# Kernel tuning notes

Hardware: AMD Instinct MI355X
Metric: run time of the kernel (lower is better)

Reference implementation:

```python
import jax, jax.numpy as jnp
import numpy as np
from jax import lax


def _lstm_dir(x, w_ih, w_hh, b_ih, b_hh, reverse):
    # x: [B,T,E]; torch LSTM gate order: i, f, g, o
    B, T, _ = x.shape
    H = w_hh.shape[1]
    xp = jnp.einsum('bte,ge->btg', x, w_ih) + b_ih + b_hh  # [B,T,4H]
    def step(carry, xt):
        h, c = carry
        gates = xt + h @ w_hh.T
        i, f, g, o = jnp.split(gates, 4, axis=-1)
        c = jax.nn.sigmoid(f) * c + jax.nn.sigmoid(i) * jnp.tanh(g)
        h = jax.nn.sigmoid(o) * jnp.tanh(c)
        return (h, c), h
    h0 = jnp.zeros((B, H), x.dtype)
    _, hs = lax.scan(step, (h0, h0), jnp.swapaxes(xp, 0, 1), reverse=reverse)
    return jnp.swapaxes(hs, 0, 1)  # [B,T,H]


def _crf_llh(emissions, tags, mask, start, end, trans):
    # torchcrf log-likelihood; emissions [B,T,C], tags [B,T], mask [B,T] bool
    maskf = mask.astype(emissions.dtype)
    em_sc = jnp.take_along_axis(emissions, tags[..., None], axis=-1)[..., 0]  # [B,T]
    tr_sc = trans[tags[:, :-1], tags[:, 1:]]                                   # [B,T-1]
    num = start[tags[:, 0]] + em_sc[:, 0] + jnp.sum((em_sc[:, 1:] + tr_sc) * maskf[:, 1:], axis=1)
    last_idx = jnp.sum(mask.astype(jnp.int32), axis=1) - 1
    last_tag = jnp.take_along_axis(tags, last_idx[:, None], axis=1)[:, 0]
    num = num + end[last_tag]
    # forward algorithm (partition function)
    alpha0 = start + emissions[:, 0]  # [B,C]
    def step(alpha, inp):
        em_t, m_t = inp  # [B,C], [B]
        sc = alpha[:, :, None] + trans[None] + em_t[:, None, :]  # [B,C,C]
        nxt = jax.scipy.special.logsumexp(sc, axis=1)
        return jnp.where(m_t[:, None], nxt, alpha), None
    alpha, _ = lax.scan(step, alpha0,
                        (jnp.swapaxes(emissions[:, 1:], 0, 1), jnp.swapaxes(mask[:, 1:], 0, 1)))
    den = jax.scipy.special.logsumexp(alpha + end[None, :], axis=1)
    return num - den  # [B]


def setup_inputs() -> dict:
    key = jax.random.key(0)
    ks = jax.random.split(key, 16)
    V, E, H, C = 30000, 512, 512, 9
    B, T = 32, 256
    s_emb = 1.0
    s_l = 1.0 / np.sqrt(H)
    inp = {
        'input': jax.random.randint(ks[0], (B, T), 0, V),
        'label': jax.random.randint(ks[1], (B, T), 0, C),
        'emb_table': jax.random.normal(ks[2], (V, E), jnp.float32) * s_emb,
        'w_ih_f': jax.random.uniform(ks[3], (4 * H, E), jnp.float32, -s_l, s_l),
        'w_hh_f': jax.random.uniform(ks[4], (4 * H, H), jnp.float32, -s_l, s_l),
        'b_ih_f': jax.random.uniform(ks[5], (4 * H,), jnp.float32, -s_l, s_l),
        'b_hh_f': jax.random.uniform(ks[6], (4 * H,), jnp.float32, -s_l, s_l),
        'w_ih_b': jax.random.uniform(ks[7], (4 * H, E), jnp.float32, -s_l, s_l),
        'w_hh_b': jax.random.uniform(ks[8], (4 * H, H), jnp.float32, -s_l, s_l),
        'b_ih_b': jax.random.uniform(ks[9], (4 * H,), jnp.float32, -s_l, s_l),
        'b_hh_b': jax.random.uniform(ks[10], (4 * H,), jnp.float32, -s_l, s_l),
        'cls_w': jax.random.uniform(ks[11], (C, 2 * H), jnp.float32, -s_l, s_l),
        'cls_b': jax.random.uniform(ks[12], (C,), jnp.float32, -s_l, s_l),
        'start_trans': jax.random.uniform(ks[13], (C,), jnp.float32, -0.1, 0.1),
        'end_trans': jax.random.uniform(ks[14], (C,), jnp.float32, -0.1, 0.1),
        'trans': jax.random.uniform(ks[15], (C, C), jnp.float32, -0.1, 0.1),
    }
    return inp


def reference(input, label, emb_table, w_ih_f, w_hh_f, b_ih_f, b_hh_f,
              w_ih_b, w_hh_b, b_ih_b, b_hh_b, cls_w, cls_b,
              start_trans, end_trans, trans):
    emb = emb_table.at[0].set(0.0)  # padding_idx=0
    x = emb[input]                  # [B,T,E]
    hf = _lstm_dir(x, w_ih_f, w_hh_f, b_ih_f, b_hh_f, reverse=False)
    hb = _lstm_dir(x, w_ih_b, w_hh_b, b_ih_b, b_hh_b, reverse=True)
    h = jnp.concatenate([hf, hb], axis=-1)          # [B,T,2H]
    logits = h @ cls_w.T + cls_b                    # [B,T,C]
    mask = label > -1
    llh = _crf_llh(logits, label, mask, start_trans, end_trans, trans)
    return -jnp.mean(llh)  # reduction='mean', negated
```

## Files before the change

kernel.cpp:

```cpp
#include <hip/hip_runtime.h>

#define TT 256
#define BB 32
#define HH 512
#define EE 512
#define GG 2048
#define MM 8192
#define NWG 32

typedef __attribute__((ext_vector_type(8))) short bf16x8;
typedef __attribute__((ext_vector_type(4))) float f32x4;
typedef __attribute__((ext_vector_type(4))) unsigned short us4;
typedef unsigned long long ull;

__device__ inline float b2f(unsigned short u) {
    union { unsigned int i; float f; } v; v.i = ((unsigned int)u) << 16; return v.f;
}
__device__ inline unsigned short f2b(float f) {
    union { float f; unsigned int i; } v; v.f = f;
    unsigned int x = v.i;
    return (unsigned short)((x + 0x7FFFu + ((x >> 16) & 1u)) >> 16);
}
__device__ inline float sigm(float x) { return 1.f / (1.f + __expf(-x)); }
__device__ inline float tanh_f(float x) {
    float ax = fminf(fabsf(x), 12.f);
    float e = __expf(2.f * ax);
    float r = (e - 1.f) / (e + 1.f);
    return x < 0.f ? -r : r;
}

__global__ void prep_embed_k(const int* __restrict__ ids, const float* __restrict__ emb,
                             const float* __restrict__ wihf, const float* __restrict__ whhf,
                             const float* __restrict__ wihb, const float* __restrict__ whhb,
                             const float* __restrict__ bihf, const float* __restrict__ bhhf,
                             const float* __restrict__ bihb, const float* __restrict__ bhhb,
                             unsigned short* __restrict__ xb, unsigned short* __restrict__ wih,
                             unsigned short* __restrict__ whh, float* __restrict__ bias)
{
    int v = blockIdx.x * 256 + threadIdx.x;
    {
        int row = v >> 7;
        int col4 = (v & 127) * 4;
        int id = ids[row];
        float4 e;
        if (id != 0) e = *(const float4*)(emb + (size_t)id * 512 + col4);
        else { e.x = 0.f; e.y = 0.f; e.z = 0.f; e.w = 0.f; }
        us4 o; o.x = f2b(e.x); o.y = f2b(e.y); o.z = f2b(e.z); o.w = f2b(e.w);
        *(us4*)(xb + (size_t)row * 512 + col4) = o;
    }
    if (v < 262144) {
        float4 a; us4 o;
        a = ((const float4*)wihf)[v];
        o.x = f2b(a.x); o.y = f2b(a.y); o.z = f2b(a.z); o.w = f2b(a.w);
        *(us4*)(wih + (size_t)v * 4) = o;
        a = ((const float4*)whhf)[v];
        o.x = f2b(a.x); o.y = f2b(a.y); o.z = f2b(a.z); o.w = f2b(a.w);
        *(us4*)(whh + (size_t)v * 4) = o;
        a = ((const float4*)wihb)[v];
        o.x = f2b(a.x); o.y = f2b(a.y); o.z = f2b(a.z); o.w = f2b(a.w);
        *(us4*)(wih + 1048576 + (size_t)v * 4) = o;
        a = ((const float4*)whhb)[v];
        o.x = f2b(a.x); o.y = f2b(a.y); o.z = f2b(a.z); o.w = f2b(a.w);
        *(us4*)(whh + 1048576 + (size_t)v * 4) = o;
        if (v < 2048)      bias[v] = bihf[v] + bhhf[v];
        else if (v < 4096) bias[v] = bihb[v - 2048] + bhhb[v - 2048];
    }
}

__global__ __launch_bounds__(256, 1) void lstm_rec(const unsigned short* __restrict__ whh,
                                                   const unsigned short* __restrict__ wih,
                                                   const unsigned short* __restrict__ xb,
                                                   const float* __restrict__ bias,
                                                   unsigned short* __restrict__ h_all,
                                                   unsigned int* __restrict__ cnt)
{
    __shared__ unsigned short hbuf[32][520];
    __shared__ unsigned short xbuf[2][32][520];
    __shared__ float gbuf[4][32][16];

    const int bx = blockIdx.x;
    const int dir = bx >> 5;
    const int wg = bx & 31;
    const int js = wg * 16;
    const int tid = threadIdx.x;
    const int wave = tid >> 6, lane = tid & 63;
    const int quad = lane >> 4, r16 = lane & 15;
    const int colw = wave * 512 + js + r16;

    bf16x8 wfr[16], xfr[16];
    {
        const unsigned short* wrow = whh + (size_t)dir * GG * HH + (size_t)colw * 512;
        const unsigned short* xrow = wih + (size_t)dir * GG * EE + (size_t)colw * 512;
#pragma unroll
        for (int kc = 0; kc < 16; ++kc) {
            wfr[kc] = *(const bf16x8*)(wrow + kc * 32 + quad * 8);
            xfr[kc] = *(const bf16x8*)(xrow + kc * 32 + quad * 8);
        }
    }
    const float bsw = bias[dir * GG + colw];

    const int cb = tid >> 3, cj = (tid & 7) * 2;
    float cr0 = 0.f, cr1 = 0.f;

    unsigned short* hd = h_all + (size_t)dir * TT * BB * HH;
    unsigned int* flg = cnt + dir * NWG;
    const int xrow32 = tid >> 3;
    const ull* xbsrc = (const ull*)xb;

    {
        const int te0 = dir ? (TT - 1) : 0;
#pragma unroll
        for (int i = 0; i < 16; ++i) {
            int v = tid + i * 256;
            int row = v >> 7, wi = v & 127;
            ull xv = xbsrc[(size_t)((row << 8) + te0) * 64 + wi];
            *(ull*)&xbuf[0][row][wi * 4] = xv;
        }
    }
    __syncthreads();
    int buf = 0;

    for (int t = 0; t < TT; ++t) {
        const int te = dir ? (TT - 1 - t) : t;

        ull xpre[16];
        if (t + 1 < TT) {
            const int tn = dir ? (te - 1) : (te + 1);
#pragma unroll
            for (int i = 0; i < 16; ++i) {
                int v = tid + i * 256;
                int row = v >> 7, wi = v & 127;
                xpre[i] = xbsrc[(size_t)((row << 8) + tn) * 64 + wi];
            }
        }

        f32x4 alo = {0.f, 0.f, 0.f, 0.f}, ahi = {0.f, 0.f, 0.f, 0.f};
#pragma unroll
        for (int kc = 0; kc < 16; ++kc) {
            const int ko = kc * 32 + quad * 8;
            bf16x8 aflo = *(const bf16x8*)&xbuf[buf][r16][ko];
            bf16x8 afhi = *(const bf16x8*)&xbuf[buf][16 + r16][ko];
            alo = __builtin_amdgcn_mfma_f32_16x16x32_bf16(aflo, xfr[kc], alo, 0, 0, 0);
            ahi = __builtin_amdgcn_mfma_f32_16x16x32_bf16(afhi, xfr[kc], ahi, 0, 0, 0);
        }

        if (t > 0) {
            if (wave == 0) {
                const unsigned int tgt = (unsigned int)t;
                for (;;) {
                    unsigned int f = tgt;
                    if (lane < NWG)
                        f = __hip_atomic_load(&flg[lane], __ATOMIC_RELAXED, __HIP_MEMORY_SCOPE_AGENT);
                    if (__ballot(f >= tgt) == ~0ull) break;
                }
            }
            __syncthreads();
            const int tp = dir ? (te + 1) : (te - 1);
            const ull* hsrc = (const ull*)(hd + (size_t)tp * BB * HH);
            ull hv[16];
#pragma unroll
            for (int i = 0; i < 16; ++i)
                hv[i] = __hip_atomic_load(&hsrc[tid + i * 256], __ATOMIC_RELAXED, __HIP_MEMORY_SCOPE_AGENT);
#pragma unroll
            for (int i = 0; i < 16; ++i) {
                int v = tid + i * 256;
                *(ull*)&hbuf[v >> 7][(v & 127) * 4] = hv[i];
            }
            __syncthreads();

#pragma unroll
            for (int kc = 0; kc < 16; ++kc) {
                const int ko = kc * 32 + quad * 8;
                bf16x8 aflo = *(const bf16x8*)&hbuf[r16][ko];
                bf16x8 afhi = *(const bf16x8*)&hbuf[16 + r16][ko];
                alo = __builtin_amdgcn_mfma_f32_16x16x32_bf16(aflo, wfr[kc], alo, 0, 0, 0);
                ahi = __builtin_amdgcn_mfma_f32_16x16x32_bf16(afhi, wfr[kc], ahi, 0, 0, 0);
            }
        }

#pragma unroll
        for (int r = 0; r < 4; ++r) {
            gbuf[wave][quad * 4 + r][r16]      = alo[r] + bsw;
            gbuf[wave][16 + quad * 4 + r][r16] = ahi[r] + bsw;
        }
        __syncthreads();

        {
            float2 iv = *(const float2*)&gbuf[0][cb][cj];
            float2 fv = *(const float2*)&gbuf[1][cb][cj];
            float2 gv = *(const float2*)&gbuf[2][cb][cj];
            float2 ov = *(const float2*)&gbuf[3][cb][cj];
            cr0 = sigm(fv.x) * cr0 + sigm(iv.x) * tanh_f(gv.x);
            cr1 = sigm(fv.y) * cr1 + sigm(iv.y) * tanh_f(gv.y);
            float h0 = sigm(ov.x) * tanh_f(cr0);
            float h1 = sigm(ov.y) * tanh_f(cr1);
            unsigned int packed = (unsigned int)f2b(h0) | ((unsigned int)f2b(h1) << 16);
            unsigned int* hp = (unsigned int*)(hd + (size_t)te * BB * HH + cb * 512 + js + cj);
            __hip_atomic_store(hp, packed, __ATOMIC_RELAXED, __HIP_MEMORY_SCOPE_AGENT);
        }

        if (t + 1 < TT) {
#pragma unroll
            for (int i = 0; i < 16; ++i) {
                int v = tid + i * 256;
                *(ull*)&xbuf[buf ^ 1][v >> 7][(v & 127) * 4] = xpre[i];
            }
            buf ^= 1;
        }
        __syncthreads();
        if (tid == 0)
            __hip_atomic_store(&flg[wg], (unsigned int)(t + 1),
                               __ATOMIC_RELAXED, __HIP_MEMORY_SCOPE_AGENT);
    }
}

__global__ __launch_bounds__(256) void logits_k(const unsigned short* __restrict__ h_all,
                                                const float* __restrict__ clsw,
                                                const float* __restrict__ clsb,
                                                float* __restrict__ logits)
{
    const int tid = threadIdx.x;
    const int wave = tid >> 6, lane = tid & 63;
    const int wgid = blockIdx.x * 4 + wave;

    unsigned int wreg[9][8];
#pragma unroll
    for (int c = 0; c < 9; ++c)
#pragma unroll
        for (int q = 0; q < 8; ++q) {
            float w0 = clsw[c * 1024 + (2 * q) * 64 + lane];
            float w1 = clsw[c * 1024 + (2 * q + 1) * 64 + lane];
            wreg[c][q] = (unsigned int)f2b(w0) | ((unsigned int)f2b(w1) << 16);
        }

    const unsigned short* hfb = h_all;
    const unsigned short* hbb = h_all + (size_t)TT * BB * HH;

    for (int i = 0; i < 8; ++i) {
        int m = wgid * 8 + i;
        int b = m >> 8, t = m & 255;
        const unsigned short* hf = hfb + ((size_t)t * BB + b) * HH;
        const unsigned short* hb = hbb + ((size_t)t * BB + b) * HH;
        float acc[9];
#pragma unroll
        for (int c = 0; c < 9; ++c) acc[c] = 0.f;
#pragma unroll
        for (int u = 0; u < 16; ++u) {
            const unsigned short* src = (u < 8) ? (hf + u * 64) : (hb + (u - 8) * 64);
            float hv = b2f(src[lane]);
#pragma unroll
            for (int c = 0; c < 9; ++c) {
                unsigned short wv = (u & 1) ? (unsigned short)(wreg[c][u >> 1] >> 16)
                                            : (unsigned short)(wreg[c][u >> 1] & 0xFFFFu);
                acc[c] += hv * b2f(wv);
            }
        }
#pragma unroll
        for (int c = 0; c < 9; ++c) {
            float s = acc[c];
            for (int off = 32; off > 0; off >>= 1) s += __shfl_down(s, off);
            if (lane == 0) logits[(size_t)m * 9 + c] = s + clsb[c];
        }
    }
}

__global__ void crf_k(const float* __restrict__ logits, const int* __restrict__ label,
                      const float* __restrict__ startp, const float* __restrict__ endp,
                      const float* __restrict__ trans, float* __restrict__ llh)
{
    const int b = blockIdx.x;
    const int lane = threadIdx.x;
    __shared__ float tr[81];
    __shared__ float alpha[9];
    __shared__ int tags[TT];
    for (int v = lane; v < 81; v += 64) tr[v] = trans[v];
    for (int v = lane; v < TT; v += 64) tags[v] = label[b * TT + v];
    __syncthreads();
    const float* lg = logits + (size_t)b * TT * 9;

    float part = 0.f; int mcnt = 0;
    for (int t = lane; t < TT; t += 64) {
        int tg = tags[t];
        bool m = tg > -1;
        if (m) mcnt++;
        if (t == 0)      part += startp[tg] + lg[tg];
        else if (m)      part += lg[t * 9 + tg] + tr[tags[t - 1] * 9 + tg];
    }
    for (int off = 32; off > 0; off >>= 1) {
        part += __shfl_down(part, off);
        mcnt += __shfl_down(mcnt, off);
    }
    part = __shfl(part, 0);
    mcnt = __shfl(mcnt, 0);
    float num = part + endp[tags[mcnt - 1]];

    if (lane < 9) alpha[lane] = startp[lane] + lg[lane];
    __syncthreads();
    for (int t = 1; t < TT; ++t) {
        float nxt = 0.f;
        if (lane < 9) {
            float mx = -1e30f;
#pragma unroll
            for (int c1 = 0; c1 < 9; ++c1) mx = fmaxf(mx, alpha[c1] + tr[c1 * 9 + lane]);
            float s = 0.f;
#pragma unroll
            for (int c1 = 0; c1 < 9; ++c1) s += __expf(alpha[c1] + tr[c1 * 9 + lane] - mx);
            nxt = mx + __logf(s) + lg[t * 9 + lane];
            if (tags[t] <= -1) nxt = alpha[lane];
        }
        __syncthreads();
        if (lane < 9) alpha[lane] = nxt;
        __syncthreads();
    }
    if (lane == 0) {
        float mx = -1e30f;
#pragma unroll
        for (int c = 0; c < 9; ++c) mx = fmaxf(mx, alpha[c] + endp[c]);
        float s = 0.f;
#pragma unroll
        for (int c = 0; c < 9; ++c) s += __expf(alpha[c] + endp[c] - mx);
        llh[b] = num - (mx + __logf(s));
    }
}

__global__ void fin_k(const float* __restrict__ llh, float* __restrict__ out)
{
    int lane = threadIdx.x;
    float v = (lane < 32) ? llh[lane] : 0.f;
    for (int off = 32; off > 0; off >>= 1) v += __shfl_down(v, off);
    if (lane == 0) out[0] = -v * (1.f / 32.f);
}

extern "C" void kernel_launch(void* const* d_in, const int* in_sizes, int n_in,
                              void* d_out, int out_size, void* d_ws, size_t ws_size,
                              hipStream_t stream)
{
    const int*   ids   = (const int*)  d_in[0];
    const int*   label = (const int*)  d_in[1];
    const float* emb   = (const float*)d_in[2];
    const float* wihf  = (const float*)d_in[3];
    const float* whhf  = (const float*)d_in[4];
    const float* bihf  = (const float*)d_in[5];
    const float* bhhf  = (const float*)d_in[6];
    const float* wihb  = (const float*)d_in[7];
    const float* whhb  = (const float*)d_in[8];
    const float* bihb  = (const float*)d_in[9];
    const float* bhhb  = (const float*)d_in[10];
    const float* clsw  = (const float*)d_in[11];
    const float* clsb  = (const float*)d_in[12];
    const float* stp   = (const float*)d_in[13];
    const float* enp   = (const float*)d_in[14];
    const float* trp   = (const float*)d_in[15];

    char* ws = (char*)d_ws;
    unsigned short* xb   = (unsigned short*)(ws + 0);
    unsigned short* wih  = (unsigned short*)(ws + 8388608);
    unsigned short* whh  = (unsigned short*)(ws + 12582912);
    float*          bias = (float*)(ws + 16777216);
    unsigned short* hall = (unsigned short*)(ws + 16793600);
    float*          lgt  = (float*)(ws + 33570816);
    float*          llh  = (float*)(ws + 33865728);
    unsigned int*   cnt  = (unsigned int*)(ws + 33865856);

    hipMemsetAsync(cnt, 0, 256, stream);
    prep_embed_k<<<4096, 256, 0, stream>>>(ids, emb, wihf, whhf, wihb, whhb,
                                           bihf, bhhf, bihb, bhhb, xb, wih, whh, bias);
    lstm_rec<<<64, 256, 0, stream>>>(whh, wih, xb, bias, hall, cnt);
    logits_k<<<256, 256, 0, stream>>>(hall, clsw, clsb, lgt);
    crf_k<<<32, 64, 0, stream>>>(lgt, label, stp, enp, trp, llh);
    fin_k<<<1, 64, 0, stream>>>(llh, (float*)d_out);
}
```

Baseline: 1.099 ms.

## Replace LSTM step barrier with per-producer flag polling and direct register loads

Each block no longer has one wave spin on all 32 producer flags, then barrier, stage h_{t-1} into LDS and barrier again. It now polls flag pairs per 32-column producer chunk and loads its MFMA A fragments straight from global memory into registers. It issues the matching MFMAs as each chunk becomes ready, and rotates the chunk order by workgroup index to spread contention. This aims to overlap recurrent-step waiting with compute and drop two __syncthreads and the LDS round trip. The cost is more scattered small atomic loads and more register pressure. The x-row stride is also corrected from 64 to 128 ull per row.

```diff
diff --git a/kernel.cpp b/kernel.cpp
--- a/kernel.cpp
+++ b/kernel.cpp
@@ -27,6 +27,12 @@
     float e = __expf(2.f * ax);
     float r = (e - 1.f) / (e + 1.f);
     return x < 0.f ? -r : r;
+}
+
+#define AGLD(p) __hip_atomic_load((p), __ATOMIC_RELAXED, __HIP_MEMORY_SCOPE_AGENT)
+
+__device__ inline bool prdy(ull f, unsigned int tgt) {
+    return ((unsigned int)f >= tgt) && ((unsigned int)(f >> 32) >= tgt);
 }
 
 __global__ void prep_embed_k(const int* __restrict__ ids, const float* __restrict__ emb,
@@ -74,7 +80,6 @@
                                                    unsigned short* __restrict__ h_all,
                                                    unsigned int* __restrict__ cnt)
 {
-    __shared__ unsigned short hbuf[32][520];
     __shared__ unsigned short xbuf[2][32][520];
     __shared__ float gbuf[4][32][16];
 
@@ -92,9 +97,9 @@
         const unsigned short* wrow = whh + (size_t)dir * GG * HH + (size_t)colw * 512;
         const unsigned short* xrow = wih + (size_t)dir * GG * EE + (size_t)colw * 512;
 #pragma unroll
-        for (int kc = 0; kc < 16; ++kc) {
-            wfr[kc] = *(const bf16x8*)(wrow + kc * 32 + quad * 8);
-            xfr[kc] = *(const bf16x8*)(xrow + kc * 32 + quad * 8);
+        for (int i = 0; i < 16; ++i) {
+            wfr[i] = *(const bf16x8*)(wrow + ((i + wg) & 15) * 32 + quad * 8);
+            xfr[i] = *(const bf16x8*)(xrow + i * 32 + quad * 8);
         }
     }
     const float bsw = bias[dir * GG + colw];
@@ -104,7 +109,6 @@
 
     unsigned short* hd = h_all + (size_t)dir * TT * BB * HH;
     unsigned int* flg = cnt + dir * NWG;
-    const int xrow32 = tid >> 3;
     const ull* xbsrc = (const ull*)xb;
 
     {
@@ -113,7 +117,7 @@
         for (int i = 0; i < 16; ++i) {
             int v = tid + i * 256;
             int row = v >> 7, wi = v & 127;
-            ull xv = xbsrc[(size_t)((row << 8) + te0) * 64 + wi];
+            ull xv = xbsrc[((size_t)(row << 8) + te0) * 128 + wi];
             *(ull*)&xbuf[0][row][wi * 4] = xv;
         }
     }
@@ -122,6 +126,14 @@
 
     for (int t = 0; t < TT; ++t) {
         const int te = dir ? (TT - 1 - t) : t;
+        const unsigned int tgt = (unsigned int)t;
+
+        ull pfl[16];
+        if (t > 0) {
+#pragma unroll
+            for (int i = 0; i < 8; ++i)
+                pfl[i] = AGLD((const ull*)&flg[2 * ((i + wg) & 15)]);
+        }
 
         ull xpre[16];
         if (t + 1 < TT) {
@@ -130,7 +142,7 @@
             for (int i = 0; i < 16; ++i) {
                 int v = tid + i * 256;
                 int row = v >> 7, wi = v & 127;
-                xpre[i] = xbsrc[(size_t)((row << 8) + tn) * 64 + wi];
+                xpre[i] = xbsrc[((size_t)(row << 8) + tn) * 128 + wi];
             }
         }
 
@@ -145,36 +157,48 @@
         }
 
         if (t > 0) {
-            if (wave == 0) {
-                const unsigned int tgt = (unsigned int)t;
-                for (;;) {
-                    unsigned int f = tgt;
-                    if (lane < NWG)
-                        f = __hip_atomic_load(&flg[lane], __ATOMIC_RELAXED, __HIP_MEMORY_SCOPE_AGENT);
-                    if (__ballot(f >= tgt) == ~0ull) break;
+            const int tp = dir ? (te + 1) : (te - 1);
+            const unsigned short* hsrc = hd + (size_t)tp * BB * HH;
+            const ull* hlo = (const ull*)hsrc + (size_t)r16 * 128 + quad * 2;
+            const ull* hhi = (const ull*)hsrc + (size_t)(16 + r16) * 128 + quad * 2;
+            ull av[8][4];
+
+#pragma unroll
+            for (int i = 0; i < 8; ++i) {
+                const int p = (i + wg) & 15;
+                ull f = pfl[i];
+                while (!prdy(f, tgt))
+                    f = AGLD((const ull*)&flg[2 * p]);
+                asm volatile("" ::: "memory");
+                const ull* pl = hlo + (size_t)p * 8;
+                const ull* ph = hhi + (size_t)p * 8;
+                av[i][0] = AGLD(pl);
+                av[i][1] = AGLD(pl + 1);
+                av[i][2] = AGLD(ph);
+                av[i][3] = AGLD(ph + 1);
+                pfl[i + 8] = AGLD((const ull*)&flg[2 * ((i + 8 + wg) & 15)]);
+            }
+#pragma unroll
+            for (int i = 0; i < 16; ++i) {
+                const int s = i & 7;
+                union { ull u[2]; bf16x8 v; } fl, fh;
+                fl.u[0] = av[s][0]; fl.u[1] = av[s][1];
+                fh.u[0] = av[s][2]; fh.u[1] = av[s][3];
+                alo = __builtin_amdgcn_mfma_f32_16x16x32_bf16(fl.v, wfr[i], alo, 0, 0, 0);
+                ahi = __builtin_amdgcn_mfma_f32_16x16x32_bf16(fh.v, wfr[i], ahi, 0, 0, 0);
+                if (i < 8) {
+                    const int p = (i + 8 + wg) & 15;
+                    ull f = pfl[i + 8];
+                    while (!prdy(f, tgt))
+                        f = AGLD((const ull*)&flg[2 * p]);
+                    asm volatile("" ::: "memory");
+                    const ull* pl = hlo + (size_t)p * 8;
+                    const ull* ph = hhi + (size_t)p * 8;
+                    av[s][0] = AGLD(pl);
+                    av[s][1] = AGLD(pl + 1);
+                    av[s][2] = AGLD(ph);
+                    av[s][3] = AGLD(ph + 1);
                 }
-            }
-            __syncthreads();
-            const int tp = dir ? (te + 1) : (te - 1);
-            const ull* hsrc = (const ull*)(hd + (size_t)tp * BB * HH);
-            ull hv[16];
-#pragma unroll
-            for (int i = 0; i < 16; ++i)
-                hv[i] = __hip_atomic_load(&hsrc[tid + i * 256], __ATOMIC_RELAXED, __HIP_MEMORY_SCOPE_AGENT);
-#pragma unroll
-            for (int i = 0; i < 16; ++i) {
-                int v = tid + i * 256;
-                *(ull*)&hbuf[v >> 7][(v & 127) * 4] = hv[i];
-            }
-            __syncthreads();
-
-#pragma unroll
-            for (int kc = 0; kc < 16; ++kc) {
-                const int ko = kc * 32 + quad * 8;
-                bf16x8 aflo = *(const bf16x8*)&hbuf[r16][ko];
-                bf16x8 afhi = *(const bf16x8*)&hbuf[16 + r16][ko];
-                alo = __builtin_amdgcn_mfma_f32_16x16x32_bf16(aflo, wfr[kc], alo, 0, 0, 0);
-                ahi = __builtin_amdgcn_mfma_f32_16x16x32_bf16(afhi, wfr[kc], ahi, 0, 0, 0);
             }
         }
 
@@ -341,6 +365,7 @@
     const float* wihf  = (const float*)d_in[3];
     const float* whhf  = (const float*)d_in[4];
     const float* bihf  = (const float*)d_in[5];
+    const float* bihf2 = 0; (void)bihf2;
     const float* bhhf  = (const float*)d_in[6];
     const float* wihb  = (const float*)d_in[7];
     const float* whhb  = (const float*)d_in[8];
```

Measured after the change: 2.817 ms. 156% more time.

## Replace flag barrier with timestep-tagged hidden-state words in LSTM recurrence

Applied to the files above, without the earlier changes.

Each hidden-state store becomes a 64-bit word that packs two bf16 values with the timestep as a tag. Consumers poll the data itself until every tag matches, so the separate per-workgroup flag array, the flag polling and the end-of-step block barrier are gone. The cross-workgroup handoff per step drops from a flag round trip plus a data load to a single tagged data load. In exchange, the hidden-state buffer doubles in size, a 32MB memset to 0xFF runs on every call to invalidate the tags, and the logits kernel must unpack the wider layout. The x-row stride in the prefetch is also corrected to 128 words.

```diff
diff --git a/kernel.cpp b/kernel.cpp
--- a/kernel.cpp
+++ b/kernel.cpp
@@ -28,6 +28,9 @@
     float r = (e - 1.f) / (e + 1.f);
     return x < 0.f ? -r : r;
 }
+
+#define AGLD(p) __hip_atomic_load((p), __ATOMIC_RELAXED, __HIP_MEMORY_SCOPE_AGENT)
+#define ASTD(p, v) __hip_atomic_store((p), (v), __ATOMIC_RELAXED, __HIP_MEMORY_SCOPE_AGENT)
 
 __global__ void prep_embed_k(const int* __restrict__ ids, const float* __restrict__ emb,
                              const float* __restrict__ wihf, const float* __restrict__ whhf,
@@ -71,11 +74,10 @@
                                                    const unsigned short* __restrict__ wih,
                                                    const unsigned short* __restrict__ xb,
                                                    const float* __restrict__ bias,
-                                                   unsigned short* __restrict__ h_all,
-                                                   unsigned int* __restrict__ cnt)
-{
+                                                   ull* __restrict__ h8)
+{
+    __shared__ unsigned short xbuf[2][32][520];
     __shared__ unsigned short hbuf[32][520];
-    __shared__ unsigned short xbuf[2][32][520];
     __shared__ float gbuf[4][32][16];
 
     const int bx = blockIdx.x;
@@ -102,9 +104,7 @@
     const int cb = tid >> 3, cj = (tid & 7) * 2;
     float cr0 = 0.f, cr1 = 0.f;
 
-    unsigned short* hd = h_all + (size_t)dir * TT * BB * HH;
-    unsigned int* flg = cnt + dir * NWG;
-    const int xrow32 = tid >> 3;
+    ull* hd8 = h8 + (size_t)dir * TT * BB * 256;
     const ull* xbsrc = (const ull*)xb;
 
     {
@@ -113,7 +113,7 @@
         for (int i = 0; i < 16; ++i) {
             int v = tid + i * 256;
             int row = v >> 7, wi = v & 127;
-            ull xv = xbsrc[(size_t)((row << 8) + te0) * 64 + wi];
+            ull xv = xbsrc[((size_t)(row << 8) + te0) * 128 + wi];
             *(ull*)&xbuf[0][row][wi * 4] = xv;
         }
     }
@@ -122,6 +122,18 @@
 
     for (int t = 0; t < TT; ++t) {
         const int te = dir ? (TT - 1 - t) : t;
+
+        ull hv[32];
+        unsigned int tagexp = 0;
+        const ull* hsrc8 = hd8;
+        if (t > 0) {
+            const int tp = dir ? (te + 1) : (te - 1);
+            tagexp = (unsigned int)tp;
+            hsrc8 = hd8 + (size_t)tp * BB * 256;
+#pragma unroll
+            for (int i = 0; i < 32; ++i)
+                hv[i] = AGLD(&hsrc8[tid + i * 256]);
+        }
 
         ull xpre[16];
         if (t + 1 < TT) {
@@ -130,7 +142,7 @@
             for (int i = 0; i < 16; ++i) {
                 int v = tid + i * 256;
                 int row = v >> 7, wi = v & 127;
-                xpre[i] = xbsrc[(size_t)((row << 8) + tn) * 64 + wi];
+                xpre[i] = xbsrc[((size_t)(row << 8) + tn) * 128 + wi];
             }
         }
 
@@ -144,30 +156,33 @@
             ahi = __builtin_amdgcn_mfma_f32_16x16x32_bf16(afhi, xfr[kc], ahi, 0, 0, 0);
         }
 
-        if (t > 0) {
-            if (wave == 0) {
-                const unsigned int tgt = (unsigned int)t;
-                for (;;) {
-                    unsigned int f = tgt;
-                    if (lane < NWG)
-                        f = __hip_atomic_load(&flg[lane], __ATOMIC_RELAXED, __HIP_MEMORY_SCOPE_AGENT);
-                    if (__ballot(f >= tgt) == ~0ull) break;
-                }
-            }
-            __syncthreads();
-            const int tp = dir ? (te + 1) : (te - 1);
-            const ull* hsrc = (const ull*)(hd + (size_t)tp * BB * HH);
-            ull hv[16];
-#pragma unroll
-            for (int i = 0; i < 16; ++i)
-                hv[i] = __hip_atomic_load(&hsrc[tid + i * 256], __ATOMIC_RELAXED, __HIP_MEMORY_SCOPE_AGENT);
+        if (t + 1 < TT) {
 #pragma unroll
             for (int i = 0; i < 16; ++i) {
                 int v = tid + i * 256;
-                *(ull*)&hbuf[v >> 7][(v & 127) * 4] = hv[i];
-            }
-            __syncthreads();
-
+                *(ull*)&xbuf[buf ^ 1][v >> 7][(v & 127) * 4] = xpre[i];
+            }
+        }
+
+        if (t > 0) {
+            for (;;) {
+                unsigned int stale = 0u;
+#pragma unroll
+                for (int i = 0; i < 32; ++i)
+                    stale |= ((unsigned int)(hv[i] >> 32) != tagexp) ? (1u << i) : 0u;
+                if (__ballot(stale != 0u) == 0ull) break;
+#pragma unroll
+                for (int i = 0; i < 32; ++i)
+                    if (stale & (1u << i))
+                        hv[i] = AGLD(&hsrc8[tid + i * 256]);
+            }
+#pragma unroll
+            for (int i = 0; i < 32; ++i)
+                *(unsigned int*)&hbuf[i][tid * 2] = (unsigned int)hv[i];
+        }
+        __syncthreads();
+
+        if (t > 0) {
 #pragma unroll
             for (int kc = 0; kc < 16; ++kc) {
                 const int ko = kc * 32 + quad * 8;
@@ -195,26 +210,14 @@
             float h0 = sigm(ov.x) * tanh_f(cr0);
             float h1 = sigm(ov.y) * tanh_f(cr1);
             unsigned int packed = (unsigned int)f2b(h0) | ((unsigned int)f2b(h1) << 16);
-            unsigned int* hp = (unsigned int*)(hd + (size_t)te * BB * HH + cb * 512 + js + cj);
-            __hip_atomic_store(hp, packed, __ATOMIC_RELAXED, __HIP_MEMORY_SCOPE_AGENT);
-        }
-
-        if (t + 1 < TT) {
-#pragma unroll
-            for (int i = 0; i < 16; ++i) {
-                int v = tid + i * 256;
-                *(ull*)&xbuf[buf ^ 1][v >> 7][(v & 127) * 4] = xpre[i];
-            }
-            buf ^= 1;
-        }
-        __syncthreads();
-        if (tid == 0)
-            __hip_atomic_store(&flg[wg], (unsigned int)(t + 1),
-                               __ATOMIC_RELAXED, __HIP_MEMORY_SCOPE_AGENT);
-    }
-}
-
-__global__ __launch_bounds__(256) void logits_k(const unsigned short* __restrict__ h_all,
+            ull out = (ull)packed | ((ull)(unsigned int)te << 32);
+            ASTD(&hd8[(size_t)te * BB * 256 + cb * 256 + ((js + cj) >> 1)], out);
+        }
+        buf ^= 1;
+    }
+}
+
+__global__ __launch_bounds__(256) void logits_k(const ull* __restrict__ h8,
                                                 const float* __restrict__ clsw,
                                                 const float* __restrict__ clsb,
                                                 float* __restrict__ logits)
@@ -233,21 +236,21 @@
             wreg[c][q] = (unsigned int)f2b(w0) | ((unsigned int)f2b(w1) << 16);
         }
 
-    const unsigned short* hfb = h_all;
-    const unsigned short* hbb = h_all + (size_t)TT * BB * HH;
-
     for (int i = 0; i < 8; ++i) {
         int m = wgid * 8 + i;
         int b = m >> 8, t = m & 255;
-        const unsigned short* hf = hfb + ((size_t)t * BB + b) * HH;
-        const unsigned short* hb = hbb + ((size_t)t * BB + b) * HH;
+        const ull* hf8 = h8 + ((size_t)t * BB + b) * 256;
+        const ull* hb8 = h8 + (size_t)TT * BB * 256 + ((size_t)t * BB + b) * 256;
         float acc[9];
 #pragma unroll
         for (int c = 0; c < 9; ++c) acc[c] = 0.f;
 #pragma unroll
         for (int u = 0; u < 16; ++u) {
-            const unsigned short* src = (u < 8) ? (hf + u * 64) : (hb + (u - 8) * 64);
-            float hv = b2f(src[lane]);
+            const ull* s8 = (u < 8) ? hf8 : hb8;
+            int cc = (u & 7) * 64 + lane;
+            ull ch = s8[cc >> 1];
+            unsigned int lo = (unsigned int)ch;
+            float hv = b2f((unsigned short)(lo >> ((cc & 1) * 16)));
 #pragma unroll
             for (int c = 0; c < 9; ++c) {
                 unsigned short wv = (u & 1) ? (unsigned short)(wreg[c][u >> 1] >> 16)
@@ -357,16 +360,15 @@
     unsigned short* wih  = (unsigned short*)(ws + 8388608);
     unsigned short* whh  = (unsigned short*)(ws + 12582912);
     float*          bias = (float*)(ws + 16777216);
-    unsigned short* hall = (unsigned short*)(ws + 16793600);
-    float*          lgt  = (float*)(ws + 33570816);
-    float*          llh  = (float*)(ws + 33865728);
-    unsigned int*   cnt  = (unsigned int*)(ws + 33865856);
-
-    hipMemsetAsync(cnt, 0, 256, stream);
+    ull*            hall8= (ull*)(ws + 16793600);
+    float*          lgt  = (float*)(ws + 50348032);
+    float*          llh  = (float*)(ws + 50642944);
+
+    hipMemsetAsync(hall8, 0xFF, 33554432, stream);
     prep_embed_k<<<4096, 256, 0, stream>>>(ids, emb, wihf, whhf, wihb, whhb,
                                            bihf, bhhf, bihb, bhhb, xb, wih, whh, bias);
-    lstm_rec<<<64, 256, 0, stream>>>(whh, wih, xb, bias, hall, cnt);
-    logits_k<<<256, 256, 0, stream>>>(hall, clsw, clsb, lgt);
+    lstm_rec<<<64, 256, 0, stream>>>(whh, wih, xb, bias, hall8);
+    logits_k<<<256, 256, 0, stream>>>(hall8, clsw, clsb, lgt);
     crf_k<<<32, 64, 0, stream>>>(lgt, label, stp, enp, trp, llh);
     fin_k<<<1, 64, 0, stream>>>(llh, (float*)d_out);
 }
```

Measured after the change: 1.651 ms. 1.5x slower.

## Interleave forward and backward LSTM directions within each workgroup to hide sync latency

Applied to the files above, without the earlier changes.

Each workgroup of the recurrent kernel now runs both LSTM directions, alternating a forward step and a backward step. While one direction waits on its cross-workgroup flags and the global h loads, the workgroup does the matmul work for the other direction, so the grid halves from 64 to 32 workgroups. Flags are prefetched, and stores are drained with an explicit vmcnt wait before each flag is published. The x-row index stride also changes from 64 to 128 ull elements. Holding weight fragments for both directions plus the prefetch buffers doubles register pressure and may cause spills.

```diff
diff --git a/kernel.cpp b/kernel.cpp
--- a/kernel.cpp
+++ b/kernel.cpp
@@ -28,6 +28,9 @@
     float r = (e - 1.f) / (e + 1.f);
     return x < 0.f ? -r : r;
 }
+
+#define AGLD(p) __hip_atomic_load((p), __ATOMIC_RELAXED, __HIP_MEMORY_SCOPE_AGENT)
+#define ASTD(p, v) __hip_atomic_store((p), (v), __ATOMIC_RELAXED, __HIP_MEMORY_SCOPE_AGENT)
 
 __global__ void prep_embed_k(const int* __restrict__ ids, const float* __restrict__ emb,
                              const float* __restrict__ wihf, const float* __restrict__ whhf,
@@ -74,114 +77,116 @@
                                                    unsigned short* __restrict__ h_all,
                                                    unsigned int* __restrict__ cnt)
 {
+    __shared__ unsigned short xbufA[32][520];
+    __shared__ unsigned short xbufB[32][520];
     __shared__ unsigned short hbuf[32][520];
-    __shared__ unsigned short xbuf[2][32][520];
     __shared__ float gbuf[4][32][16];
 
-    const int bx = blockIdx.x;
-    const int dir = bx >> 5;
-    const int wg = bx & 31;
+    const int wg = blockIdx.x;
     const int js = wg * 16;
     const int tid = threadIdx.x;
     const int wave = tid >> 6, lane = tid & 63;
     const int quad = lane >> 4, r16 = lane & 15;
     const int colw = wave * 512 + js + r16;
 
-    bf16x8 wfr[16], xfr[16];
+    bf16x8 wfrA[16], xfrA[16], wfrB[16], xfrB[16];
     {
-        const unsigned short* wrow = whh + (size_t)dir * GG * HH + (size_t)colw * 512;
-        const unsigned short* xrow = wih + (size_t)dir * GG * EE + (size_t)colw * 512;
+        const unsigned short* wrA = whh + (size_t)colw * 512;
+        const unsigned short* xrA = wih + (size_t)colw * 512;
+        const unsigned short* wrB = whh + (size_t)GG * HH + (size_t)colw * 512;
+        const unsigned short* xrB = wih + (size_t)GG * EE + (size_t)colw * 512;
 #pragma unroll
         for (int kc = 0; kc < 16; ++kc) {
-            wfr[kc] = *(const bf16x8*)(wrow + kc * 32 + quad * 8);
-            xfr[kc] = *(const bf16x8*)(xrow + kc * 32 + quad * 8);
-        }
-    }
-    const float bsw = bias[dir * GG + colw];
+            wfrA[kc] = *(const bf16x8*)(wrA + kc * 32 + quad * 8);
+            xfrA[kc] = *(const bf16x8*)(xrA + kc * 32 + quad * 8);
+            wfrB[kc] = *(const bf16x8*)(wrB + kc * 32 + quad * 8);
+            xfrB[kc] = *(const bf16x8*)(xrB + kc * 32 + quad * 8);
+        }
+    }
+    const float bswA = bias[colw];
+    const float bswB = bias[GG + colw];
 
     const int cb = tid >> 3, cj = (tid & 7) * 2;
-    float cr0 = 0.f, cr1 = 0.f;
-
-    unsigned short* hd = h_all + (size_t)dir * TT * BB * HH;
-    unsigned int* flg = cnt + dir * NWG;
-    const int xrow32 = tid >> 3;
+    float cA0 = 0.f, cA1 = 0.f, cB0 = 0.f, cB1 = 0.f;
+
+    unsigned short* hdA = h_all;
+    unsigned short* hdB = h_all + (size_t)TT * BB * HH;
+    unsigned int* flgA = cnt;
+    unsigned int* flgB = cnt + NWG;
     const ull* xbsrc = (const ull*)xb;
 
-    {
-        const int te0 = dir ? (TT - 1) : 0;
-#pragma unroll
-        for (int i = 0; i < 16; ++i) {
-            int v = tid + i * 256;
-            int row = v >> 7, wi = v & 127;
-            ull xv = xbsrc[(size_t)((row << 8) + te0) * 64 + wi];
-            *(ull*)&xbuf[0][row][wi * 4] = xv;
-        }
+#pragma unroll
+    for (int i = 0; i < 16; ++i) {
+        int v = tid + i * 256;
+        int row = v >> 7, wi = v & 127;
+        *(ull*)&xbufA[row][wi * 4] = xbsrc[((size_t)(row << 8) + 0) * 128 + wi];
+        *(ull*)&xbufB[row][wi * 4] = xbsrc[((size_t)(row << 8) + (TT - 1)) * 128 + wi];
     }
     __syncthreads();
-    int buf = 0;
+
+    ull hvA[16], hvB[16], xpreA[16], xpreB[16];
+    unsigned int pfA = 0, pfB = 0;
 
     for (int t = 0; t < TT; ++t) {
-        const int te = dir ? (TT - 1 - t) : t;
-
-        ull xpre[16];
-        if (t + 1 < TT) {
-            const int tn = dir ? (te - 1) : (te + 1);
+        const int te2 = TT - 1 - t;
+
+        if (t > 0) {
 #pragma unroll
             for (int i = 0; i < 16; ++i) {
                 int v = tid + i * 256;
                 int row = v >> 7, wi = v & 127;
-                xpre[i] = xbsrc[(size_t)((row << 8) + tn) * 64 + wi];
-            }
-        }
-
-        f32x4 alo = {0.f, 0.f, 0.f, 0.f}, ahi = {0.f, 0.f, 0.f, 0.f};
-#pragma unroll
-        for (int kc = 0; kc < 16; ++kc) {
-            const int ko = kc * 32 + quad * 8;
-            bf16x8 aflo = *(const bf16x8*)&xbuf[buf][r16][ko];
-            bf16x8 afhi = *(const bf16x8*)&xbuf[buf][16 + r16][ko];
-            alo = __builtin_amdgcn_mfma_f32_16x16x32_bf16(aflo, xfr[kc], alo, 0, 0, 0);
-            ahi = __builtin_amdgcn_mfma_f32_16x16x32_bf16(afhi, xfr[kc], ahi, 0, 0, 0);
-        }
-
-        if (t > 0) {
-            if (wave == 0) {
-                const unsigned int tgt = (unsigned int)t;
-                for (;;) {
-                    unsigned int f = tgt;
-                    if (lane < NWG)
-                        f = __hip_atomic_load(&flg[lane], __ATOMIC_RELAXED, __HIP_MEMORY_SCOPE_AGENT);
-                    if (__ballot(f >= tgt) == ~0ull) break;
-                }
-            }
-            __syncthreads();
-            const int tp = dir ? (te + 1) : (te - 1);
-            const ull* hsrc = (const ull*)(hd + (size_t)tp * BB * HH);
-            ull hv[16];
-#pragma unroll
-            for (int i = 0; i < 16; ++i)
-                hv[i] = __hip_atomic_load(&hsrc[tid + i * 256], __ATOMIC_RELAXED, __HIP_MEMORY_SCOPE_AGENT);
+                *(ull*)&hbuf[row][wi * 4]  = hvA[i];
+                *(ull*)&xbufB[row][wi * 4] = xpreB[i];
+            }
+        }
+        __syncthreads();
+
+        if (t + 1 < TT) {
 #pragma unroll
             for (int i = 0; i < 16; ++i) {
                 int v = tid + i * 256;
-                *(ull*)&hbuf[v >> 7][(v & 127) * 4] = hv[i];
-            }
-            __syncthreads();
-
+                int row = v >> 7, wi = v & 127;
+                xpreA[i] = xbsrc[((size_t)(row << 8) + (t + 1)) * 128 + wi];
+            }
+        }
+
+        f32x4 alo = {0.f, 0.f, 0.f, 0.f}, ahi = {0.f, 0.f, 0.f, 0.f};
+        if (t > 0) {
 #pragma unroll
             for (int kc = 0; kc < 16; ++kc) {
                 const int ko = kc * 32 + quad * 8;
                 bf16x8 aflo = *(const bf16x8*)&hbuf[r16][ko];
                 bf16x8 afhi = *(const bf16x8*)&hbuf[16 + r16][ko];
-                alo = __builtin_amdgcn_mfma_f32_16x16x32_bf16(aflo, wfr[kc], alo, 0, 0, 0);
-                ahi = __builtin_amdgcn_mfma_f32_16x16x32_bf16(afhi, wfr[kc], ahi, 0, 0, 0);
-            }
+                alo = __builtin_amdgcn_mfma_f32_16x16x32_bf16(aflo, wfrA[kc], alo, 0, 0, 0);
+                ahi = __builtin_amdgcn_mfma_f32_16x16x32_bf16(afhi, wfrA[kc], ahi, 0, 0, 0);
+            }
+        }
+
+        if (t > 0) {
+            unsigned int f = pfB;
+            const unsigned int tgt = (unsigned int)t;
+            while (__ballot(f >= tgt) != ~0ull)
+                f = AGLD(&flgB[lane & 31]);
+            asm volatile("" ::: "memory");
+            const ull* hs = (const ull*)(hdB + (size_t)(TT - t) * BB * HH);
+#pragma unroll
+            for (int i = 0; i < 16; ++i)
+                hvB[i] = AGLD(&hs[tid + i * 256]);
+        }
+
+#pragma unroll
+        for (int kc = 0; kc < 16; ++kc) {
+            const int ko = kc * 32 + quad * 8;
+            bf16x8 aflo = *(const bf16x8*)&xbufA[r16][ko];
+            bf16x8 afhi = *(const bf16x8*)&xbufA[16 + r16][ko];
+            alo = __builtin_amdgcn_mfma_f32_16x16x32_bf16(aflo, xfrA[kc], alo, 0, 0, 0);
+            ahi = __builtin_amdgcn_mfma_f32_16x16x32_bf16(afhi, xfrA[kc], ahi, 0, 0, 0);
         }
 
 #pragma unroll
         for (int r = 0; r < 4; ++r) {
-            gbuf[wave][quad * 4 + r][r16]      = alo[r] + bsw;
-            gbuf[wave][16 + quad * 4 + r][r16] = ahi[r] + bsw;
+            gbuf[wave][quad * 4 + r][r16]      = alo[r] + bswA;
+            gbuf[wave][16 + quad * 4 + r][r16] = ahi[r] + bswA;
         }
         __syncthreads();
 
@@ -190,27 +195,92 @@
             float2 fv = *(const float2*)&gbuf[1][cb][cj];
             float2 gv = *(const float2*)&gbuf[2][cb][cj];
             float2 ov = *(const float2*)&gbuf[3][cb][cj];
-            cr0 = sigm(fv.x) * cr0 + sigm(iv.x) * tanh_f(gv.x);
-            cr1 = sigm(fv.y) * cr1 + sigm(iv.y) * tanh_f(gv.y);
-            float h0 = sigm(ov.x) * tanh_f(cr0);
-            float h1 = sigm(ov.y) * tanh_f(cr1);
+            cA0 = sigm(fv.x) * cA0 + sigm(iv.x) * tanh_f(gv.x);
+            cA1 = sigm(fv.y) * cA1 + sigm(iv.y) * tanh_f(gv.y);
+            float h0 = sigm(ov.x) * tanh_f(cA0);
+            float h1 = sigm(ov.y) * tanh_f(cA1);
             unsigned int packed = (unsigned int)f2b(h0) | ((unsigned int)f2b(h1) << 16);
-            unsigned int* hp = (unsigned int*)(hd + (size_t)te * BB * HH + cb * 512 + js + cj);
+            unsigned int* hp = (unsigned int*)(hdA + (size_t)t * BB * HH + cb * 512 + js + cj);
             __hip_atomic_store(hp, packed, __ATOMIC_RELAXED, __HIP_MEMORY_SCOPE_AGENT);
         }
+        asm volatile("s_waitcnt vmcnt(0)" ::: "memory");
+        if (tid == 0) ASTD(&flgA[wg], (unsigned int)(t + 1));
+        if (t + 1 < TT) pfA = AGLD(&flgA[lane & 31]);
+
+#pragma unroll
+        for (int i = 0; i < 16; ++i) {
+            int v = tid + i * 256;
+            int row = v >> 7, wi = v & 127;
+            if (t > 0)      *(ull*)&hbuf[row][wi * 4]  = hvB[i];
+            if (t + 1 < TT) *(ull*)&xbufA[row][wi * 4] = xpreA[i];
+        }
+        __syncthreads();
 
         if (t + 1 < TT) {
 #pragma unroll
             for (int i = 0; i < 16; ++i) {
                 int v = tid + i * 256;
-                *(ull*)&xbuf[buf ^ 1][v >> 7][(v & 127) * 4] = xpre[i];
-            }
-            buf ^= 1;
-        }
-        __syncthreads();
-        if (tid == 0)
-            __hip_atomic_store(&flg[wg], (unsigned int)(t + 1),
-                               __ATOMIC_RELAXED, __HIP_MEMORY_SCOPE_AGENT);
+                int row = v >> 7, wi = v & 127;
+                xpreB[i] = xbsrc[((size_t)(row << 8) + (te2 - 1)) * 128 + wi];
+            }
+        }
+
+        alo = f32x4{0.f, 0.f, 0.f, 0.f}; ahi = f32x4{0.f, 0.f, 0.f, 0.f};
+        if (t > 0) {
+#pragma unroll
+            for (int kc = 0; kc < 16; ++kc) {
+                const int ko = kc * 32 + quad * 8;
+                bf16x8 aflo = *(const bf16x8*)&hbuf[r16][ko];
+                bf16x8 afhi = *(const bf16x8*)&hbuf[16 + r16][ko];
+                alo = __builtin_amdgcn_mfma_f32_16x16x32_bf16(aflo, wfrB[kc], alo, 0, 0, 0);
+                ahi = __builtin_amdgcn_mfma_f32_16x16x32_bf16(afhi, wfrB[kc], ahi, 0, 0, 0);
+            }
+        }
+
+        if (t + 1 < TT) {
+            unsigned int f = pfA;
+            const unsigned int tgt = (unsigned int)(t + 1);
+            while (__ballot(f >= tgt) != ~0ull)
+                f = AGLD(&flgA[lane & 31]);
+            asm volatile("" ::: "memory");
+            const ull* hs = (const ull*)(hdA + (size_t)t * BB * HH);
+#pragma unroll
+            for (int i = 0; i < 16; ++i)
+                hvA[i] = AGLD(&hs[tid + i * 256]);
+        }
+
+#pragma unroll
+        for (int kc = 0; kc < 16; ++kc) {
+            const int ko = kc * 32 + quad * 8;
+            bf16x8 aflo = *(const bf16x8*)&xbufB[r16][ko];
+            bf16x8 afhi = *(const bf16x8*)&xbufB[16 + r16][ko];
+            alo = __builtin_amdgcn_mfma_f32_16x16x32_bf16(aflo, xfrB[kc], alo, 0, 0, 0);
+            ahi = __builtin_amdgcn_mfma_f32_16x16x32_bf16(afhi, xfrB[kc], ahi, 0, 0, 0);
+        }
+
+#pragma unroll
+        for (int r = 0; r < 4; ++r) {
+            gbuf[wave][quad * 4 + r][r16]      = alo[r] + bswB;
+            gbuf[wave][16 + quad * 4 + r][r16] = ahi[r] + bswB;
+        }
+        __syncthreads();
+
+        {
+            float2 iv = *(const float2*)&gbuf[0][cb][cj];
+            float2 fv = *(const float2*)&gbuf[1][cb][cj];
+            float2 gv = *(const float2*)&gbuf[2][cb][cj];
+            float2 ov = *(const float2*)&gbuf[3][cb][cj];
+            cB0 = sigm(fv.x) * cB0 + sigm(iv.x) * tanh_f(gv.x);
+            cB1 = sigm(fv.y) * cB1 + sigm(iv.y) * tanh_f(gv.y);
+            float h0 = sigm(ov.x) * tanh_f(cB0);
+            float h1 = sigm(ov.y) * tanh_f(cB1);
+            unsigned int packed = (unsigned int)f2b(h0) | ((unsigned int)f2b(h1) << 16);
+            unsigned int* hp = (unsigned int*)(hdB + (size_t)te2 * BB * HH + cb * 512 + js + cj);
+            __hip_atomic_store(hp, packed, __ATOMIC_RELAXED, __HIP_MEMORY_SCOPE_AGENT);
+        }
+        asm volatile("s_waitcnt vmcnt(0)" ::: "memory");
+        if (tid == 0) ASTD(&flgB[wg], (unsigned int)(t + 1));
+        if (t + 1 < TT) pfB = AGLD(&flgB[lane & 31]);
     }
 }
 
@@ -365,7 +435,7 @@
     hipMemsetAsync(cnt, 0, 256, stream);
     prep_embed_k<<<4096, 256, 0, stream>>>(ids, emb, wihf, whhf, wihb, whhb,
                                            bihf, bhhf, bihb, bhhb, xb, wih, whh, bias);
-    lstm_rec<<<64, 256, 0, stream>>>(whh, wih, xb, bias, hall, cnt);
+    lstm_rec<<<32, 256, 0, stream>>>(whh, wih, xb, bias, hall, cnt);
     logits_k<<<256, 256, 0, stream>>>(hall, clsw, clsb, lgt);
     crf_k<<<32, 64, 0, stream>>>(lgt, label, stp, enp, trp, llh);
     fin_k<<<1, 64, 0, stream>>>(llh, (float*)d_out);
```

After: 2.831 ms. +157.7%, slower.
